# Performance work log

Measured on AMD Instinct MI355X. Metric: run time of the kernel, lower is better.

Reference implementation:

```python
import jax, jax.numpy as jnp
import numpy as np

B, S, D = 2, 2048, 1024
N_HEADS, D_HEAD = 16, 64
INIT_STD = 0.02


def setup_inputs() -> dict:
    key = jax.random.key(0)
    k_res, k_q, k_k, k_v, k_o = jax.random.split(key, 5)
    residual = jax.random.normal(k_res, (B, S, D), dtype=jnp.float32)
    W_Q = INIT_STD * jax.random.normal(k_q, (N_HEADS, D_HEAD, D), dtype=jnp.float32)
    W_K = INIT_STD * jax.random.normal(k_k, (N_HEADS, D_HEAD, D), dtype=jnp.float32)
    W_V = INIT_STD * jax.random.normal(k_v, (N_HEADS, D_HEAD, D), dtype=jnp.float32)
    W_O = INIT_STD * jax.random.normal(k_o, (N_HEADS, D_HEAD, D), dtype=jnp.float32)
    return {"residual": residual, "W_Q": W_Q, "W_K": W_K, "W_V": W_V, "W_O": W_O}


def reference(residual, W_Q, W_K, W_V, W_O):
    seq_len = residual.shape[1]
    # projections: [b, n, p, h]  (heads first, matching q.transpose(1,2))
    q = jnp.einsum('bpd,nhd->bnph', residual, W_Q)
    k = jnp.einsum('bpd,nhd->bnph', residual, W_K)
    v = jnp.einsum('bpd,nhd->bnph', residual, W_V)
    scale = 1.0 / jnp.sqrt(jnp.asarray(q.shape[-1], dtype=residual.dtype))
    # [b, n, p_q, p_k] full score matrix (faithful to original naive impl)
    scores = jnp.einsum('bnqh,bnkh->bnqk', q, k) * scale
    causal = jnp.tril(jnp.ones((seq_len, seq_len), dtype=bool))
    scores = jnp.where(causal, scores, -jnp.inf)
    pattern = jax.nn.softmax(scores, axis=-1)
    attn_out = jnp.einsum('bnqk,bnkh->bnqh', pattern, v)
    # output projection summed over heads: 'bpnh,nhd->bpd'
    return jnp.einsum('bnph,nhd->bpd', attn_out, W_O)
```

## Files before the change

### kernel.cpp

```cpp
#include <hip/hip_runtime.h>
#include <math.h>


#define SS_ 2048
#define DD_ 1024
#define NH_ 16
#define BN_ 32
#define BS_ 4096

typedef __bf16 bf16x8 __attribute__((ext_vector_type(8)));
typedef __bf16 bf16x4 __attribute__((ext_vector_type(4)));
typedef short shortx4 __attribute__((ext_vector_type(4)));
typedef float floatx4 __attribute__((ext_vector_type(4)));
typedef unsigned short ushortx4 __attribute__((ext_vector_type(4)));

__device__ __forceinline__ unsigned short f2bf(float f) {
    union { float f; unsigned u; } v; v.f = f;
    unsigned r = v.u + 0x7FFFu + ((v.u >> 16) & 1u);
    return (unsigned short)(r >> 16);
}

__device__ __forceinline__ floatx4 mfma_pv(bf16x4 a, bf16x4 b, floatx4 c) {
#if __has_builtin(__builtin_amdgcn_mfma_f32_16x16x16_bf16)
    return __builtin_amdgcn_mfma_f32_16x16x16_bf16(a, b, c, 0, 0, 0);
#else
    return __builtin_amdgcn_mfma_f32_16x16x16bf16_1k(
        __builtin_bit_cast(shortx4, a), __builtin_bit_cast(shortx4, b), c, 0, 0, 0);
#endif
}

__device__ __forceinline__ void gl_lds16(const unsigned short* g, unsigned short* l) {
    __builtin_amdgcn_global_load_lds(
        (const __attribute__((address_space(1))) unsigned int*)g,
        (__attribute__((address_space(3))) unsigned int*)l, 16, 0, 0);
}

__global__ __launch_bounds__(256) void cast_bf16_kernel(
    const float* __restrict__ resid, const float* __restrict__ WQ,
    const float* __restrict__ WK, const float* __restrict__ WV,
    unsigned short* __restrict__ residB, unsigned short* __restrict__ WQb,
    unsigned short* __restrict__ WKb, unsigned short* __restrict__ WVb)
{
    const int z = blockIdx.y;
    if (z > 0 && blockIdx.x >= 1024) return;
    const float* src = (z == 0) ? resid : (z == 1) ? WQ : (z == 2) ? WK : WV;
    unsigned short* dst = (z == 0) ? residB : (z == 1) ? WQb : (z == 2) ? WKb : WVb;
    const int i = (blockIdx.x * 256 + threadIdx.x) * 4;
    float4 f = *(const float4*)(src + i);
    ushortx4 o;
    o[0] = f2bf(f.x); o[1] = f2bf(f.y); o[2] = f2bf(f.z); o[3] = f2bf(f.w);
    *(ushortx4*)(dst + i) = o;
}

__global__ __launch_bounds__(256) void wo_transpose_kernel(
    const float* __restrict__ WO, unsigned short* __restrict__ WOt)
{
    __shared__ float t[64][65];
    const int kk0 = blockIdx.x * 64, d0 = blockIdx.y * 64;
    #pragma unroll
    for (int it = 0; it < 16; ++it) {
        int idx = it * 256 + threadIdx.x;
        int r = idx >> 6, c = idx & 63;
        t[r][c] = WO[(kk0 + r) * DD_ + d0 + c];
    }
    __syncthreads();
    #pragma unroll
    for (int it = 0; it < 16; ++it) {
        int idx = it * 256 + threadIdx.x;
        int r = idx >> 6, c = idx & 63;
        WOt[(d0 + r) * DD_ + kk0 + c] = f2bf(t[c][r]);
    }
}

__global__ __launch_bounds__(256) void qkv_m97_kernel(
    const unsigned short* __restrict__ residB,
    const unsigned short* __restrict__ WQb,
    const unsigned short* __restrict__ WKb,
    const unsigned short* __restrict__ WVb,
    unsigned short* __restrict__ q, unsigned short* __restrict__ kk,
    unsigned short* __restrict__ vT)
{
    __shared__ unsigned short As[128 * 64];
    __shared__ unsigned short Bs[128 * 64];
    const int tid = threadIdx.x;
    const int l = tid & 63, w = tid >> 6;
    const int quad = l >> 4, lan = l & 15;
    const int z = blockIdx.z;
    const unsigned short* W = (z == 0) ? WQb : (z == 1) ? WKb : WVb;
    unsigned short* dst = (z == 0) ? q : (z == 1) ? kk : vT;
    const int mBase = blockIdx.x * 128;
    const int nBase = blockIdx.y * 128;
    const int wm = (w & 1) * 64, wn = (w >> 1) * 64;

    floatx4 acc[4][4];
    #pragma unroll
    for (int a = 0; a < 4; ++a)
        #pragma unroll
        for (int b = 0; b < 4; ++b)
            #pragma unroll
            for (int i = 0; i < 4; ++i) acc[a][b][i] = 0.f;

    const int sr = l >> 3;
    const int sgx = ((l & 7) ^ sr) * 8;

    for (int k0 = 0; k0 < DD_; k0 += 64) {
        __syncthreads();
        #pragma unroll
        for (int i = 0; i < 4; ++i) {
            const int row = i * 32 + w * 8 + sr;
            gl_lds16(residB + (size_t)(mBase + row) * DD_ + k0 + sgx,
                     As + i * 2048 + w * 512);
            gl_lds16(W + (size_t)(nBase + row) * DD_ + k0 + sgx,
                     Bs + i * 2048 + w * 512);
        }
        __syncthreads();
        #pragma unroll
        for (int ks = 0; ks < 2; ++ks) {
            const int fo = (((ks * 4 + quad) ^ (lan & 7)) << 3);
            bf16x8 a[4], b[4];
            #pragma unroll
            for (int mi = 0; mi < 4; ++mi)
                a[mi] = *(const bf16x8*)(As + (wm + mi * 16 + lan) * 64 + fo);
            #pragma unroll
            for (int ni = 0; ni < 4; ++ni)
                b[ni] = *(const bf16x8*)(Bs + (wn + ni * 16 + lan) * 64 + fo);
            #pragma unroll
            for (int mi = 0; mi < 4; ++mi)
                #pragma unroll
                for (int ni = 0; ni < 4; ++ni)
                    acc[mi][ni] = __builtin_amdgcn_mfma_f32_16x16x32_bf16(
                        a[mi], b[ni], acc[mi][ni], 0, 0, 0);
        }
    }
    const int headU = (nBase + wn) >> 6;
    const float scale = (z == 0) ? 0.125f * 1.44269504088896340736f : 1.0f;
    if (z < 2) {
        #pragma unroll
        for (int mi = 0; mi < 4; ++mi)
            #pragma unroll
            for (int ni = 0; ni < 4; ++ni)
                #pragma unroll
                for (int reg = 0; reg < 4; ++reg) {
                    int m = mBase + wm + mi * 16 + quad * 4 + reg;
                    int bb = m >> 11, ss = m & 2047;
                    int h = ni * 16 + lan;
                    dst[((size_t)(bb * NH_ + headU) * SS_ + ss) * 64 + h] =
                        f2bf(acc[mi][ni][reg] * scale);
                }
    } else {
        #pragma unroll
        for (int mi = 0; mi < 4; ++mi) {
            const int m0 = mBase + wm + mi * 16 + quad * 4;
            const int bb = m0 >> 11, ss0 = m0 & 2047;
            #pragma unroll
            for (int ni = 0; ni < 4; ++ni) {
                const int h = ni * 16 + lan;
                bf16x4 ob;
                #pragma unroll
                for (int reg = 0; reg < 4; ++reg)
                    ob[reg] = static_cast<__bf16>(acc[mi][ni][reg]);
                *(bf16x4*)(dst + ((size_t)(bb * NH_ + headU) * 64 + h) * SS_ + ss0) = ob;
            }
        }
    }
}

__global__ __launch_bounds__(256, 4) void flash_mfma_kernel(
    const unsigned short* __restrict__ q,
    const unsigned short* __restrict__ k,
    const unsigned short* __restrict__ vT,
    unsigned short* __restrict__ attn)
{
    __shared__ unsigned short ldsK[3][64 * 64];
    __shared__ unsigned short ldsV[2][64 * 64];
    const int l = threadIdx.x & 63, w = threadIdx.x >> 6;
    const int quad = l >> 4, lan = l & 15;
    const int f = blockIdx.x;
    const int bn = (f & 7) | (((f >> 3) & 3) << 3);
    const int chunk = 31 - (f >> 5);

    const unsigned short* Qg = q  + (size_t)bn * SS_ * 64;
    const unsigned short* Kg = k  + (size_t)bn * SS_ * 64;
    const unsigned short* Vg = vT + (size_t)bn * 64 * SS_;

    const int srl = l >> 3;
    const int sgx = (l & 7) ^ srl;

    const int qRow0 = chunk * 64 + w * 16;
    const int qAbs = qRow0 + lan;

    const unsigned short* Qr = Qg + (size_t)qAbs * 64 + quad * 8;
    bf16x8 Qf0 = *(const bf16x8*)(Qr);
    bf16x8 Qf1 = *(const bf16x8*)(Qr + 32);

    bf16x4 ones;
    #pragma unroll
    for (int i = 0; i < 4; ++i) ones[i] = static_cast<__bf16>(1.0f);

    float mrow = -INFINITY;
    floatx4 l_acc;
    floatx4 o[4];
    #pragma unroll
    for (int i = 0; i < 4; ++i) l_acc[i] = 0.f;
    #pragma unroll
    for (int t = 0; t < 4; ++t)
        #pragma unroll
        for (int i = 0; i < 4; ++i) o[t][i] = 0.f;

    #define STAGE_K(kt_, buf_)                                                  \
        { const int row0_ = w * 16, kB_ = (kt_) * 64;                           \
          gl_lds16(Kg + (size_t)(kB_ + row0_ + srl) * 64 + sgx * 8,             \
                   &ldsK[buf_][row0_ * 64]);                                    \
          gl_lds16(Kg + (size_t)(kB_ + row0_ + 8 + srl) * 64 + sgx * 8,         \
                   &ldsK[buf_][(row0_ + 8) * 64]); }
    #define STAGE_V(kt_, buf_)                                                  \
        { const int row0_ = w * 16, kB_ = (kt_) * 64;                           \
          gl_lds16(Vg + (size_t)(row0_ + srl) * SS_ + kB_ + sgx * 8,            \
                   &ldsV[buf_][row0_ * 64]);                                    \
          gl_lds16(Vg + (size_t)(row0_ + 8 + srl) * SS_ + kB_ + sgx * 8,        \
                   &ldsV[buf_][(row0_ + 8) * 64]); }
    #define QK_TILE(dst_, buf_)                                                 \
        { const unsigned short* Kb_ = &ldsK[buf_][0];                           \
          _Pragma("unroll")                                                     \
          for (int nt = 0; nt < 4; ++nt) {                                      \
              const unsigned short* kr_ = Kb_ + (nt * 16 + lan) * 64;           \
              bf16x8 K0_ = *(const bf16x8*)(kr_ + ((quad ^ (lan & 7)) << 3));   \
              bf16x8 K1_ = *(const bf16x8*)(kr_ + (((quad + 4) ^ (lan & 7)) << 3)); \
              floatx4 zz_; zz_[0] = zz_[1] = zz_[2] = zz_[3] = 0.f;             \
              dst_[nt] = __builtin_amdgcn_mfma_f32_16x16x32_bf16(K0_, Qf0, zz_, 0, 0, 0); \
              dst_[nt] = __builtin_amdgcn_mfma_f32_16x16x32_bf16(K1_, Qf1, dst_[nt], 0, 0, 0); } }

    STAGE_K(0, 0);
    STAGE_V(0, 0);
    __syncthreads();
    if (chunk >= 1) STAGE_K(1, 1);
    floatx4 scCur[4], scNext[4];
    QK_TILE(scCur, 0);

    for (int kt = 0; kt <= chunk; ++kt) {
        const int kBase = kt * 64;
        __syncthreads();
        if (kt + 2 <= chunk) STAGE_K(kt + 2, (kt + 2) % 3);
        if (kt + 1 <= chunk) {
            STAGE_V(kt + 1, (kt + 1) & 1);
            QK_TILE(scNext, (kt + 1) % 3);
        }
        if (kt == chunk) {
            #pragma unroll
            for (int nt = 0; nt < 4; ++nt)
                #pragma unroll
                for (int reg = 0; reg < 4; ++reg)
                    if (kBase + nt * 16 + quad * 4 + reg > qAbs)
                        scCur[nt][reg] = -INFINITY;
        }
        float mx = scCur[0][0];
        #pragma unroll
        for (int nt = 0; nt < 4; ++nt)
            #pragma unroll
            for (int reg = 0; reg < 4; ++reg) mx = fmaxf(mx, scCur[nt][reg]);
        mx = fmaxf(mx, __shfl_xor(mx, 16, 64));
        mx = fmaxf(mx, __shfl_xor(mx, 32, 64));
        const float mnew = fmaxf(mrow, mx);
        if (!__all(mx <= mrow)) {
            const float alpha = exp2f(mrow - mnew);
            l_acc[0] *= alpha;
            #pragma unroll
            for (int t = 0; t < 4; ++t)
                #pragma unroll
                for (int i = 0; i < 4; ++i) o[t][i] *= alpha;
        }
        mrow = mnew;
        bf16x4 pb[4];
        #pragma unroll
        for (int nt = 0; nt < 4; ++nt)
            #pragma unroll
            for (int reg = 0; reg < 4; ++reg)
                pb[nt][reg] = static_cast<__bf16>(exp2f(scCur[nt][reg] - mnew));
        #pragma unroll
        for (int nt = 0; nt < 4; ++nt)
            l_acc = mfma_pv(ones, pb[nt], l_acc);
        const unsigned short* Vb = &ldsV[kt & 1][0];
        #pragma unroll
        for (int t = 0; t < 4; ++t) {
            const unsigned short* vr = Vb + (t * 16 + lan) * 64 + ((quad & 1) << 2);
            #pragma unroll
            for (int nt = 0; nt < 4; ++nt) {
                const int g = nt * 2 + (quad >> 1);
                bf16x4 Vf = *(const bf16x4*)(vr + ((g ^ (lan & 7)) << 3));
                o[t] = mfma_pv(Vf, pb[nt], o[t]);
            }
        }
        #pragma unroll
        for (int nt = 0; nt < 4; ++nt) scCur[nt] = scNext[nt];
    }
    const float rl = 1.f / l_acc[0];
    #pragma unroll
    for (int t = 0; t < 4; ++t) {
        bf16x4 ob;
        #pragma unroll
        for (int reg = 0; reg < 4; ++reg)
            ob[reg] = static_cast<__bf16>(o[t][reg] * rl);
        *(bf16x4*)(attn + ((size_t)bn * SS_ + qAbs) * 64 + t * 16 + quad * 4) = ob;
    }
    #undef STAGE_K
    #undef STAGE_V
    #undef QK_TILE
}

__global__ __launch_bounds__(256) void out_m97_kernel(
    const unsigned short* __restrict__ attn,
    const unsigned short* __restrict__ WOt,
    float* __restrict__ out)
{
    __shared__ unsigned short As[128 * 64];
    __shared__ unsigned short Bs[128 * 64];
    const int tid = threadIdx.x;
    const int l = tid & 63, w = tid >> 6;
    const int quad = l >> 4, lan = l & 15;
    const int mBase = blockIdx.x * 128;
    const int nBase = blockIdx.y * 128;
    const int wm = (w & 1) * 64, wn = (w >> 1) * 64;
    const int bbU = mBase >> 11;
    const int ssBase = mBase & 2047;

    floatx4 acc[4][4];
    #pragma unroll
    for (int a = 0; a < 4; ++a)
        #pragma unroll
        for (int b = 0; b < 4; ++b)
            #pragma unroll
            for (int i = 0; i < 4; ++i) acc[a][b][i] = 0.f;

    const int sr = l >> 3;
    const int sgx = ((l & 7) ^ sr) * 8;

    for (int kt = 0; kt < 16; ++kt) {
        const int k0 = kt * 64;
        __syncthreads();
        #pragma unroll
        for (int i = 0; i < 4; ++i) {
            const int row = i * 32 + w * 8 + sr;
            gl_lds16(attn + ((size_t)(bbU * NH_ + kt) * SS_ + ssBase + row) * 64 + sgx,
                     As + i * 2048 + w * 512);
            gl_lds16(WOt + (size_t)(nBase + row) * DD_ + k0 + sgx,
                     Bs + i * 2048 + w * 512);
        }
        __syncthreads();
        #pragma unroll
        for (int ks = 0; ks < 2; ++ks) {
            const int fo = (((ks * 4 + quad) ^ (lan & 7)) << 3);
            bf16x8 a[4], b[4];
            #pragma unroll
            for (int mi = 0; mi < 4; ++mi)
                a[mi] = *(const bf16x8*)(As + (wm + mi * 16 + lan) * 64 + fo);
            #pragma unroll
            for (int ni = 0; ni < 4; ++ni)
                b[ni] = *(const bf16x8*)(Bs + (wn + ni * 16 + lan) * 64 + fo);
            #pragma unroll
            for (int mi = 0; mi < 4; ++mi)
                #pragma unroll
                for (int ni = 0; ni < 4; ++ni)
                    acc[mi][ni] = __builtin_amdgcn_mfma_f32_16x16x32_bf16(
                        a[mi], b[ni], acc[mi][ni], 0, 0, 0);
        }
    }
    #pragma unroll
    for (int mi = 0; mi < 4; ++mi)
        #pragma unroll
        for (int ni = 0; ni < 4; ++ni)
            #pragma unroll
            for (int reg = 0; reg < 4; ++reg) {
                int m = mBase + wm + mi * 16 + quad * 4 + reg;
                out[(size_t)m * DD_ + nBase + wn + ni * 16 + lan] = acc[mi][ni][reg];
            }
}

extern "C" void kernel_launch(void* const* d_in, const int* in_sizes, int n_in,
                              void* d_out, int out_size, void* d_ws, size_t ws_size,
                              hipStream_t stream) {
    const float* resid = (const float*)d_in[0];
    const float* WQ    = (const float*)d_in[1];
    const float* WK    = (const float*)d_in[2];
    const float* WV    = (const float*)d_in[3];
    const float* WO    = (const float*)d_in[4];
    float* out = (float*)d_out;

    unsigned short* q      = (unsigned short*)d_ws;
    unsigned short* kk     = q      + 4194304;
    unsigned short* vT     = kk     + 4194304;
    unsigned short* attn   = vT     + 4194304;
    unsigned short* residB = attn   + 4194304;
    unsigned short* WQb    = residB + 4194304;
    unsigned short* WKb    = WQb    + 1048576;
    unsigned short* WVb    = WKb    + 1048576;
    unsigned short* WOt    = WVb    + 1048576;

    cast_bf16_kernel<<<dim3(4096, 4), 256, 0, stream>>>(
        resid, WQ, WK, WV, residB, WQb, WKb, WVb);
    wo_transpose_kernel<<<dim3(16, 16), 256, 0, stream>>>(WO, WOt);
    qkv_m97_kernel<<<dim3(32, 8, 3), 256, 0, stream>>>(
        residB, WQb, WKb, WVb, q, kk, vT);
    flash_mfma_kernel<<<dim3(1024), dim3(256), 0, stream>>>(q, kk, vT, attn);
    out_m97_kernel<<<dim3(32, 8), 256, 0, stream>>>(attn, WOt, out);
}
```

Measured before the change: 194.0 us.

## Use 128-row query blocks with 8 waves and deeper triple-buffered K/V pipeline

The flash attention kernel now launches 512 blocks of 512 threads, each handling 128 query rows with 8 waves, so every K/V tile staged in LDS serves twice as many queries. V gets a third LDS buffer and K/V are prefetched further ahead. Explicit s_waitcnt with vmcnt(2) plus raw barriers replace __syncthreads so outstanding loads can stay in flight. Chunk ordering is remapped to balance the causal workload. Larger blocks may reduce occupancy, and the hand-written waitcnt counts risk ordering bugs.

Result: slower. 204.0 us (+5.2%).

```diff
diff --git a/kernel.cpp b/kernel.cpp
--- a/kernel.cpp
+++ b/kernel.cpp
@@ -165,19 +165,21 @@
     }
 }
 
-__global__ __launch_bounds__(256, 4) void flash_mfma_kernel(
+__global__ __launch_bounds__(512, 4) void flash_mfma_kernel(
     const unsigned short* __restrict__ q,
     const unsigned short* __restrict__ k,
     const unsigned short* __restrict__ vT,
     unsigned short* __restrict__ attn)
 {
     __shared__ unsigned short ldsK[3][64 * 64];
-    __shared__ unsigned short ldsV[2][64 * 64];
+    __shared__ unsigned short ldsV[3][64 * 64];
     const int l = threadIdx.x & 63, w = threadIdx.x >> 6;
     const int quad = l >> 4, lan = l & 15;
     const int f = blockIdx.x;
     const int bn = (f & 7) | (((f >> 3) & 3) << 3);
-    const int chunk = 31 - (f >> 5);
+    const int g = f >> 5;
+    const int c = (g < 8) ? (15 - g) : (g - 8);
+    const int nit = 2 * c + 2;
 
     const unsigned short* Qg = q  + (size_t)bn * SS_ * 64;
     const unsigned short* Kg = k  + (size_t)bn * SS_ * 64;
@@ -186,8 +188,7 @@
     const int srl = l >> 3;
     const int sgx = (l & 7) ^ srl;
 
-    const int qRow0 = chunk * 64 + w * 16;
-    const int qAbs = qRow0 + lan;
+    const int qAbs = c * 128 + w * 16 + lan;
 
     const unsigned short* Qr = Qg + (size_t)qAbs * 64 + quad * 8;
     bf16x8 Qf0 = *(const bf16x8*)(Qr);
@@ -208,17 +209,11 @@
         for (int i = 0; i < 4; ++i) o[t][i] = 0.f;
 
     #define STAGE_K(kt_, buf_)                                                  \
-        { const int row0_ = w * 16, kB_ = (kt_) * 64;                           \
-          gl_lds16(Kg + (size_t)(kB_ + row0_ + srl) * 64 + sgx * 8,             \
-                   &ldsK[buf_][row0_ * 64]);                                    \
-          gl_lds16(Kg + (size_t)(kB_ + row0_ + 8 + srl) * 64 + sgx * 8,         \
-                   &ldsK[buf_][(row0_ + 8) * 64]); }
+        gl_lds16(Kg + (size_t)((kt_) * 64 + w * 8 + srl) * 64 + sgx * 8,        \
+                 &ldsK[buf_][w * 8 * 64]);
     #define STAGE_V(kt_, buf_)                                                  \
-        { const int row0_ = w * 16, kB_ = (kt_) * 64;                           \
-          gl_lds16(Vg + (size_t)(row0_ + srl) * SS_ + kB_ + sgx * 8,            \
-                   &ldsV[buf_][row0_ * 64]);                                    \
-          gl_lds16(Vg + (size_t)(row0_ + 8 + srl) * SS_ + kB_ + sgx * 8,        \
-                   &ldsV[buf_][(row0_ + 8) * 64]); }
+        gl_lds16(Vg + (size_t)(w * 8 + srl) * SS_ + (kt_) * 64 + sgx * 8,       \
+                 &ldsV[buf_][w * 8 * 64]);
     #define QK_TILE(dst_, buf_)                                                 \
         { const unsigned short* Kb_ = &ldsK[buf_][0];                           \
           _Pragma("unroll")                                                     \
@@ -232,20 +227,28 @@
 
     STAGE_K(0, 0);
     STAGE_V(0, 0);
-    __syncthreads();
-    if (chunk >= 1) STAGE_K(1, 1);
+    STAGE_K(1, 1);
+    asm volatile("s_waitcnt vmcnt(0) lgkmcnt(0)" ::: "memory");
+    __builtin_amdgcn_s_barrier();
+    asm volatile("" ::: "memory");
+    { const int t2 = (2 < nit) ? 2 : nit - 1; STAGE_K(t2, 2); }
+    STAGE_V(1, 1);
     floatx4 scCur[4], scNext[4];
     QK_TILE(scCur, 0);
 
-    for (int kt = 0; kt <= chunk; ++kt) {
+    for (int kt = 0; kt < nit; ++kt) {
         const int kBase = kt * 64;
-        __syncthreads();
-        if (kt + 2 <= chunk) STAGE_K(kt + 2, (kt + 2) % 3);
-        if (kt + 1 <= chunk) {
-            STAGE_V(kt + 1, (kt + 1) & 1);
+        asm volatile("s_waitcnt vmcnt(2) lgkmcnt(0)" ::: "memory");
+        __builtin_amdgcn_s_barrier();
+        asm volatile("" ::: "memory");
+        { const int tk = (kt + 3 < nit) ? kt + 3 : nit - 1;
+          STAGE_K(tk, (kt + 3) % 3); }
+        { const int tv = (kt + 2 < nit) ? kt + 2 : nit - 1;
+          STAGE_V(tv, (kt + 2) % 3); }
+        if (kt + 1 < nit) {
             QK_TILE(scNext, (kt + 1) % 3);
         }
-        if (kt == chunk) {
+        if (kt >= nit - 2) {
             #pragma unroll
             for (int nt = 0; nt < 4; ++nt)
                 #pragma unroll
@@ -279,20 +282,23 @@
         #pragma unroll
         for (int nt = 0; nt < 4; ++nt)
             l_acc = mfma_pv(ones, pb[nt], l_acc);
-        const unsigned short* Vb = &ldsV[kt & 1][0];
+        const unsigned short* Vb = &ldsV[kt % 3][0];
         #pragma unroll
         for (int t = 0; t < 4; ++t) {
             const unsigned short* vr = Vb + (t * 16 + lan) * 64 + ((quad & 1) << 2);
             #pragma unroll
             for (int nt = 0; nt < 4; ++nt) {
-                const int g = nt * 2 + (quad >> 1);
-                bf16x4 Vf = *(const bf16x4*)(vr + ((g ^ (lan & 7)) << 3));
+                const int g2 = nt * 2 + (quad >> 1);
+                bf16x4 Vf = *(const bf16x4*)(vr + ((g2 ^ (lan & 7)) << 3));
                 o[t] = mfma_pv(Vf, pb[nt], o[t]);
             }
         }
-        #pragma unroll
-        for (int nt = 0; nt < 4; ++nt) scCur[nt] = scNext[nt];
-    }
+        if (kt + 1 < nit) {
+            #pragma unroll
+            for (int nt = 0; nt < 4; ++nt) scCur[nt] = scNext[nt];
+        }
+    }
+    asm volatile("s_waitcnt vmcnt(0)" ::: "memory");
     const float rl = 1.f / l_acc[0];
     #pragma unroll
     for (int t = 0; t < 4; ++t) {
@@ -400,6 +406,6 @@
     wo_transpose_kernel<<<dim3(16, 16), 256, 0, stream>>>(WO, WOt);
     qkv_m97_kernel<<<dim3(32, 8, 3), 256, 0, stream>>>(
         residB, WQb, WKb, WVb, q, kk, vT);
-    flash_mfma_kernel<<<dim3(1024), dim3(256), 0, stream>>>(q, kk, vT, attn);
+    flash_mfma_kernel<<<dim3(512), dim3(512), 0, stream>>>(q, kk, vT, attn);
     out_m97_kernel<<<dim3(32, 8), 256, 0, stream>>>(attn, WOt, out);
 }
```
